# Performance work log

Hardware: AMD Instinct MI355X
Metric: run time of the kernel (lower is better)

## Reference

```python
import jax, jax.numpy as jnp
import numpy as np

D_K = 64


def setup_inputs() -> dict:
    key = jax.random.key(0)
    kq, kk, kv, km = jax.random.split(key, 4)
    B, H, S = 4, 16, 2048
    Q = jax.random.normal(kq, (B, H, S, D_K), dtype=jnp.float32)
    K = jax.random.normal(kk, (B, H, S, D_K), dtype=jnp.float32)
    V = jax.random.normal(kv, (B, H, S, D_K), dtype=jnp.float32)
    # boolean mask, True = masked out; broadcast over heads
    mask = jax.random.randint(km, (B, 1, S, S), 0, 2).astype(jnp.bool_)
    return {"Q": Q, "K": K, "V": V, "mask": mask}


def reference(Q, K, V, mask):
    scale = jnp.sqrt(jnp.asarray(D_K, dtype=Q.dtype))
    # [B,H,S,S] scores
    scores = jnp.einsum('bhqd,bhkd->bhqk', Q, K) / scale
    scores = jnp.where(mask, jnp.asarray(-1e9, dtype=scores.dtype), scores)
    attn = jax.nn.softmax(scores, axis=-1)
    return jnp.einsum('bhqk,bhkd->bhqd', attn, V)
```

## Files before the change

### kernel.cpp

```cpp
#include <hip/hip_runtime.h>
#include <hip/hip_bf16.h>


#define SEQ   2048
#define DK    64
#define NB_   4
#define NBH   64
#define KVB   64
#define QB    128
#define NT    (SEQ / KVB)

#define MASKH_WORDS ((size_t)NB_ * SEQ * 64)
#define WSK_OFF ((size_t)2 * 1024 * 1024)
#define WSV_OFF ((size_t)18 * 1024 * 1024)
#define WS_NEED ((size_t)34 * 1024 * 1024)

typedef float    f32x16 __attribute__((ext_vector_type(16)));
typedef _Float16 f16x8  __attribute__((ext_vector_type(8)));
typedef _Float16 f16x2v __attribute__((ext_vector_type(2)));

#define QSCALE 0.18033688011112042f
#define MINIT  (-1.0e4f)

#if __has_builtin(__builtin_amdgcn_exp2f)
#define EXP2F(x) __builtin_amdgcn_exp2f(x)
#else
__device__ __forceinline__ float EXP2F(float x) {
  float r;
  asm("v_exp_f32 %0, %1\n\ts_nop 1" : "=v"(r) : "v"(x));
  return r;
}
#endif

__device__ __forceinline__ unsigned pkrtz(float lo, float hi) {
  auto v = __builtin_amdgcn_cvt_pkrtz(lo, hi);
  return __builtin_bit_cast(unsigned, v);
}

#define GLOAD16(g, l)                                                          \
  __builtin_amdgcn_global_load_lds(                                            \
      (const __attribute__((address_space(1))) unsigned*)(g),                  \
      (__attribute__((address_space(3))) unsigned*)(l), 16, 0, 0)

#define BARRIER()                                          \
  do {                                                     \
    asm volatile("s_waitcnt lgkmcnt(0)" ::: "memory");     \
    __builtin_amdgcn_s_barrier();                          \
  } while (0)

__device__ __forceinline__ void halfswap(unsigned a, unsigned b,
                                         unsigned& out_lo, unsigned& out_hi, int hiL) {
#if __has_builtin(__builtin_amdgcn_permlane32_swap)
  auto r = __builtin_amdgcn_permlane32_swap(a, b, false, false);
  out_lo = r[0];
  out_hi = r[1];
#else
  unsigned ax = __shfl_xor(a, 32), bx = __shfl_xor(b, 32);
  out_lo = hiL ? bx : a;
  out_hi = hiL ? b : ax;
#endif
}

__global__ __launch_bounds__(256) void pre_all(
    const int* __restrict__ M, const float* __restrict__ K,
    const float* __restrict__ V, unsigned* __restrict__ Mh,
    _Float16* __restrict__ wsK, _Float16* __restrict__ wsV) {
  const int blk = blockIdx.x;
  if (blk < 2048) {
    int t  = blk * 256 + threadIdx.x;
    int hi = t & 1, T = (t >> 1) & 31, q = (t >> 6) & 2047, b = t >> 17;
    const int* src = M + ((size_t)b * SEQ + q) * SEQ + T * 64 + 4 * hi;
    unsigned bits = 0;
#pragma unroll
    for (int kvb = 0; kvb < 2; ++kvb)
#pragma unroll
      for (int m = 0; m < 4; ++m) {
        int4 v = *(const int4*)(src + 32 * kvb + 8 * m);
        int sh = 16 * kvb + 4 * m;
        bits |= ((unsigned)(v.x != 0) << sh) | ((unsigned)(v.y != 0) << (sh + 1)) |
                ((unsigned)(v.z != 0) << (sh + 2)) | ((unsigned)(v.w != 0) << (sh + 3));
      }
    Mh[t] = bits;
  } else if (blk < 6144) {
    int t  = (blk - 2048) * 256 + threadIdx.x;
    int lq = t & 31, c = (t >> 5) & 15, kt = (t >> 9) & 31, bh = t >> 14;
    int kv = kt * 64 + (c >> 3) * 32 + lq;
    int d0 = ((c >> 1) & 3) * 16 + (c & 1) * 8;
    const float4* src = (const float4*)(K + ((size_t)bh * SEQ + kv) * DK + d0);
    float4 a = src[0], b4 = src[1];
    uint4 o = { pkrtz(a.x, a.y), pkrtz(a.z, a.w), pkrtz(b4.x, b4.y), pkrtz(b4.z, b4.w) };
    *(uint4*)(wsK + (size_t)t * 8) = o;
  } else {
    int t  = (blk - 6144) * 256 + threadIdx.x;
    int lq = t & 31, c = (t >> 5) & 15, kt = (t >> 9) & 31, bh = t >> 14;
    int kv0 = kt * 64 + ((c >> 1) & 3) * 16 + (c & 1) * 8;
    int d   = (c >> 3) * 32 + lq;
    const float* vp = V + ((size_t)bh * SEQ + kv0) * DK + d;
    float v[8];
#pragma unroll
    for (int j = 0; j < 8; ++j) v[j] = vp[(size_t)j * DK];
    uint4 o = { pkrtz(v[0], v[1]), pkrtz(v[2], v[3]), pkrtz(v[4], v[5]), pkrtz(v[6], v[7]) };
    *(uint4*)(wsV + (size_t)t * 8) = o;
  }
}


__global__ __launch_bounds__(256) void sda_attn_pc(
    const float* __restrict__ Q, const unsigned* __restrict__ Mh,
    const _Float16* __restrict__ wsK, const _Float16* __restrict__ wsV,
    float* __restrict__ O) {
  __shared__ __align__(16) _Float16 Kl[2][16 * 256];
  __shared__ __align__(16) _Float16 Vt[2][16 * 256];

  const int bh   = blockIdx.x;
  const int qt   = blockIdx.y;
  const int b    = bh >> 4;
  const int tid  = threadIdx.x;
  const int wid  = tid >> 6;
  const int lane = tid & 63;
  const int lq   = lane & 31;
  const int hiL  = lane >> 5;

  const size_t base = (size_t)bh * SEQ * DK;
  const int    q    = qt * QB + wid * 32 + lq;

  f16x8 qf[4];
  {
    const float* qp = Q + base + (size_t)q * DK + hiL * 8;
#pragma unroll
    for (int kk = 0; kk < 4; ++kk) {
      float4 A  = *(const float4*)(qp + kk * 16);
      float4 Bv = *(const float4*)(qp + kk * 16 + 4);
      uint4 u;
      u.x = pkrtz(A.x * QSCALE, A.y * QSCALE);
      u.y = pkrtz(A.z * QSCALE, A.w * QSCALE);
      u.z = pkrtz(Bv.x * QSCALE, Bv.y * QSCALE);
      u.w = pkrtz(Bv.z * QSCALE, Bv.w * QSCALE);
      qf[kk] = __builtin_bit_cast(f16x8, u);
    }
  }

  f32x16 oacc[2];
#pragma unroll
  for (int db = 0; db < 2; ++db)
#pragma unroll
    for (int r = 0; r < 16; ++r) oacc[db][r] = 0.f;
  float lreg = 0.f;

  const _Float16* skb = wsK + (size_t)bh * 32 * 4096 + wid * 1024 + lane * 8;
  const _Float16* svb = wsV + (size_t)bh * 32 * 4096 + wid * 1024 + lane * 8;

#define STAGE_GL(buf_, kt_)                                   \
  {                                                           \
    const _Float16* sk = skb + (size_t)(kt_) * 4096;          \
    const _Float16* sv = svb + (size_t)(kt_) * 4096;          \
    _Float16* dk = &Kl[buf_][wid * 1024];                     \
    _Float16* dv = &Vt[buf_][wid * 1024];                     \
    GLOAD16(sk, dk);                                          \
    GLOAD16(sk + 512, dk + 512);                              \
    GLOAD16(sv, dv);                                          \
    GLOAD16(sv + 512, dv + 512);                              \
  }

  const unsigned* Mhp = Mh + ((size_t)b * SEQ + q) * 64 + hiL;
  const f16x2v ones = {(_Float16)1.0f, (_Float16)1.0f};
  (void)ones;

  STAGE_GL(0, 0);
  unsigned mw_cur = Mhp[0];
  asm volatile("s_waitcnt vmcnt(0)" ::: "memory");
  BARRIER();

  for (int t = 0; t < NT; ++t) {
    const int  cur  = t & 1;
    const bool more = (t + 1 < NT);
    unsigned mw_next = 0;
    if (more) {
      STAGE_GL(cur ^ 1, t + 1);
      mw_next = Mhp[2 * (t + 1)];
    }

    f32x16 sc[2];
#pragma unroll
    for (int kvb = 0; kvb < 2; ++kvb)
#pragma unroll
      for (int r = 0; r < 16; ++r)
        sc[kvb][r] = (mw_cur & (1u << (16 * kvb + r))) ? MINIT : 0.f;

    __builtin_amdgcn_s_setprio(1);
#pragma unroll
    for (int kk = 0; kk < 4; ++kk)
#pragma unroll
      for (int kvb = 0; kvb < 2; ++kvb) {
        f16x8 kf = *(const f16x8*)&Kl[cur][(kvb * 8 + kk * 2 + hiL) * 256 + lq * 8];
        sc[kvb] = __builtin_amdgcn_mfma_f32_32x32x16_f16(kf, qf[kk], sc[kvb], 0, 0, 0);
      }
    __builtin_amdgcn_s_setprio(0);

    float rs0 = 0.f, rs1 = 0.f;
    unsigned pr[2][4][2];
#pragma unroll
    for (int kvb = 0; kvb < 2; ++kvb)
#pragma unroll
      for (int m = 0; m < 4; ++m) {
        float e0 = EXP2F(sc[kvb][4 * m + 0]);
        float e1 = EXP2F(sc[kvb][4 * m + 1]);
        float e2 = EXP2F(sc[kvb][4 * m + 2]);
        float e3 = EXP2F(sc[kvb][4 * m + 3]);
        unsigned w0 = pkrtz(e0, e1);
        unsigned w1 = pkrtz(e2, e3);
        pr[kvb][m][0] = w0;
        pr[kvb][m][1] = w1;
#if __has_builtin(__builtin_amdgcn_fdot2)
        rs0 = __builtin_amdgcn_fdot2(__builtin_bit_cast(f16x2v, w0), ones, rs0, false);
        rs1 = __builtin_amdgcn_fdot2(__builtin_bit_cast(f16x2v, w1), ones, rs1, false);
#else
        rs0 += e0 + e1;
        rs1 += e2 + e3;
#endif
      }
    float rs = rs0 + rs1;

    {
      unsigned ru = __builtin_bit_cast(unsigned, rs), plo, phi;
      halfswap(ru, ru, plo, phi, hiL);
      float other = __builtin_bit_cast(float, hiL ? plo : phi);
      lreg += rs + other;
    }

#pragma unroll
    for (int ks = 0; ks < 4; ++ks) {
      const int kvb = ks >> 1, ms = (ks & 1) * 2;
      unsigned w0, w1, w2, w3;
      halfswap(pr[kvb][ms][0], pr[kvb][ms + 1][0], w0, w2, hiL);
      halfswap(pr[kvb][ms][1], pr[kvb][ms + 1][1], w1, w3, hiL);
      f16x8 pf = __builtin_bit_cast(f16x8, make_uint4(w0, w1, w2, w3));

      __builtin_amdgcn_s_setprio(1);
#pragma unroll
      for (int db = 0; db < 2; ++db) {
        f16x8 vf = *(const f16x8*)&Vt[cur][(db * 8 + ks * 2 + hiL) * 256 + lq * 8];
        oacc[db] = __builtin_amdgcn_mfma_f32_32x32x16_f16(vf, pf, oacc[db], 0, 0, 0);
      }
      __builtin_amdgcn_s_setprio(0);
    }

    mw_cur = mw_next;
    if (more) {
      asm volatile("s_waitcnt vmcnt(0)" ::: "memory");
      BARRIER();
    }
  }

  float inv = (lreg > 0.f) ? 1.0f / lreg : 0.f;
  float* op = O + base + (size_t)q * DK + 4 * hiL;
#pragma unroll
  for (int db = 0; db < 2; ++db)
#pragma unroll
    for (int m = 0; m < 4; ++m) {
      float4 o;
      o.x = oacc[db][4 * m + 0] * inv;
      o.y = oacc[db][4 * m + 1] * inv;
      o.z = oacc[db][4 * m + 2] * inv;
      o.w = oacc[db][4 * m + 3] * inv;
      *(float4*)(op + 32 * db + 8 * m) = o;
    }
}


#define CH 264
__global__ __launch_bounds__(256) void sda_attn_fb(
    const float* __restrict__ Q, const float* __restrict__ K,
    const float* __restrict__ V, const int* __restrict__ M,
    float* __restrict__ O) {
  __shared__ __align__(16) _Float16 Kl[2][16 * CH];
  __shared__ __align__(16) _Float16 Vt[2][16 * CH];
  const int bh = blockIdx.x, qt = blockIdx.y, b = bh >> 4;
  const int tid = threadIdx.x, wid = tid >> 6, lane = tid & 63;
  const int lq = lane & 31, hiL = lane >> 5;
  const size_t base = (size_t)bh * SEQ * DK;
  const int q = qt * QB + wid * 32 + lq;

  f16x8 qf[4];
  {
    const float* qp = Q + base + (size_t)q * DK + hiL * 8;
#pragma unroll
    for (int kk = 0; kk < 4; ++kk) {
      float4 A = *(const float4*)(qp + kk * 16), Bv = *(const float4*)(qp + kk * 16 + 4);
      uint4 u = { pkrtz(A.x * QSCALE, A.y * QSCALE), pkrtz(A.z * QSCALE, A.w * QSCALE),
                  pkrtz(Bv.x * QSCALE, Bv.y * QSCALE), pkrtz(Bv.z * QSCALE, Bv.w * QSCALE) };
      qf[kk] = __builtin_bit_cast(f16x8, u);
    }
  }
  f32x16 oacc[2];
#pragma unroll
  for (int db = 0; db < 2; ++db)
#pragma unroll
    for (int r = 0; r < 16; ++r) oacc[db][r] = 0.f;
  float lreg = 0.f;

  const int krow = tid >> 2, c0 = tid & 3, kp = tid & 31, d8 = (tid >> 5) * 8;
  const float* Kg = K + base + (size_t)krow * DK + c0 * 16;
  const float* Vg0 = V + base + (size_t)(2 * kp) * DK + d8;
  const float* Vg1 = Vg0 + DK;
  const int kwa = ((krow >> 5) * 8 + c0 * 2) * CH + (krow & 31) * 8;
  const int kwb = kwa + CH;
  const int vwb = ((d8 >> 5) * 8 + (kp >> 3) * 2 + ((kp >> 2) & 1)) * CH +
                  (d8 & 31) * 8 + (kp & 3) * 2;
  float4 kpre[4], vpre[4];
#define FLOADT(kb_)                                                      \
  {                                                                      \
    const float* kg = Kg + (size_t)(kb_)*DK;                             \
    _Pragma("unroll") for (int i = 0; i < 4; ++i)                        \
        kpre[i] = *(const float4*)(kg + 4 * i);                          \
    const float* va = Vg0 + (size_t)(kb_)*DK;                            \
    const float* vb = Vg1 + (size_t)(kb_)*DK;                            \
    vpre[0] = *(const float4*)va; vpre[1] = *(const float4*)(va + 4);    \
    vpre[2] = *(const float4*)vb; vpre[3] = *(const float4*)(vb + 4);    \
  }
#define FSTAGE(b_)                                                          \
  {                                                                         \
    uint4 u0, u1;                                                           \
    u0.x = pkrtz(kpre[0].x, kpre[0].y); u0.y = pkrtz(kpre[0].z, kpre[0].w); \
    u0.z = pkrtz(kpre[1].x, kpre[1].y); u0.w = pkrtz(kpre[1].z, kpre[1].w); \
    u1.x = pkrtz(kpre[2].x, kpre[2].y); u1.y = pkrtz(kpre[2].z, kpre[2].w); \
    u1.z = pkrtz(kpre[3].x, kpre[3].y); u1.w = pkrtz(kpre[3].z, kpre[3].w); \
    *(uint4*)&Kl[b_][kwa] = u0;                                             \
    *(uint4*)&Kl[b_][kwb] = u1;                                             \
    const float* va_ = (const float*)&vpre[0];                              \
    const float* vc_ = (const float*)&vpre[2];                              \
    _Pragma("unroll") for (int j = 0; j < 8; ++j)                           \
        *(unsigned*)&Vt[b_][vwb + j * 8] = pkrtz(va_[j], vc_[j]);           \
  }
  const int* Mrow = M + ((size_t)b * SEQ + q) * SEQ + 4 * hiL;
  FLOADT(0); FSTAGE(0); FLOADT(KVB);
  BARRIER();
  for (int t = 0; t < NT; ++t) {
    const int cur = t & 1;
    f32x16 sc[2];
#pragma unroll
    for (int kvb = 0; kvb < 2; ++kvb)
#pragma unroll
      for (int r = 0; r < 16; ++r) sc[kvb][r] = 0.f;
#pragma unroll
    for (int kk = 0; kk < 4; ++kk)
#pragma unroll
      for (int kvb = 0; kvb < 2; ++kvb) {
        f16x8 kf = *(const f16x8*)&Kl[cur][(kvb * 8 + kk * 2 + hiL) * CH + lq * 8];
        sc[kvb] = __builtin_amdgcn_mfma_f32_32x32x16_f16(kf, qf[kk], sc[kvb], 0, 0, 0);
      }
    const bool more = (t + 1 < NT);
    if (more) { FSTAGE(cur ^ 1); if (t + 2 < NT) FLOADT((t + 2) * KVB); }
    int4 mraw[8];
#pragma unroll
    for (int kvb = 0; kvb < 2; ++kvb)
#pragma unroll
      for (int m = 0; m < 4; ++m)
        mraw[kvb * 4 + m] = *(const int4*)(Mrow + t * KVB + 32 * kvb + 8 * m);
    float rs = 0.f;
    unsigned pr[2][4][2];
#pragma unroll
    for (int kvb = 0; kvb < 2; ++kvb) {
      float e[16];
#pragma unroll
      for (int r = 0; r < 16; ++r) {
        float ev = EXP2F(sc[kvb][r]);
        int4 v = mraw[kvb * 4 + (r >> 2)];
        int mm = (r & 3) == 0 ? v.x : (r & 3) == 1 ? v.y : (r & 3) == 2 ? v.z : v.w;
        ev = mm != 0 ? 0.f : ev;
        e[r] = ev; rs += ev;
      }
#pragma unroll
      for (int m = 0; m < 4; ++m) {
        pr[kvb][m][0] = pkrtz(e[4 * m + 0], e[4 * m + 1]);
        pr[kvb][m][1] = pkrtz(e[4 * m + 2], e[4 * m + 3]);
      }
    }
    {
      unsigned ru = __builtin_bit_cast(unsigned, rs), plo, phi;
      halfswap(ru, ru, plo, phi, hiL);
      lreg += rs + __builtin_bit_cast(float, hiL ? plo : phi);
    }
#pragma unroll
    for (int ks = 0; ks < 4; ++ks) {
      const int kvb = ks >> 1, ms = (ks & 1) * 2;
      unsigned w0, w1, w2, w3;
      halfswap(pr[kvb][ms][0], pr[kvb][ms + 1][0], w0, w2, hiL);
      halfswap(pr[kvb][ms][1], pr[kvb][ms + 1][1], w1, w3, hiL);
      f16x8 pf = __builtin_bit_cast(f16x8, make_uint4(w0, w1, w2, w3));
#pragma unroll
      for (int db = 0; db < 2; ++db) {
        f16x8 vf = *(const f16x8*)&Vt[cur][(db * 8 + ks * 2 + hiL) * CH + lq * 8];
        oacc[db] = __builtin_amdgcn_mfma_f32_32x32x16_f16(vf, pf, oacc[db], 0, 0, 0);
      }
    }
    if (more) BARRIER();
  }
  float inv = (lreg > 0.f) ? 1.0f / lreg : 0.f;
  float* op = O + base + (size_t)q * DK + 4 * hiL;
#pragma unroll
  for (int db = 0; db < 2; ++db)
#pragma unroll
    for (int m = 0; m < 4; ++m) {
      float4 o;
      o.x = oacc[db][4 * m + 0] * inv;
      o.y = oacc[db][4 * m + 1] * inv;
      o.z = oacc[db][4 * m + 2] * inv;
      o.w = oacc[db][4 * m + 3] * inv;
      *(float4*)(op + 32 * db + 8 * m) = o;
    }
}

extern "C" void kernel_launch(void* const* d_in, const int* in_sizes, int n_in,
                              void* d_out, int out_size, void* d_ws, size_t ws_size,
                              hipStream_t stream) {
  const float* Q = (const float*)d_in[0];
  const float* K = (const float*)d_in[1];
  const float* V = (const float*)d_in[2];
  const int*   M = (const int*)d_in[3];
  float*       O = (float*)d_out;
  dim3 grid(NBH, SEQ / QB);

  if (ws_size >= WS_NEED) {
    unsigned*  Mh  = (unsigned*)d_ws;
    _Float16*  wsK = (_Float16*)((char*)d_ws + WSK_OFF);
    _Float16*  wsV = (_Float16*)((char*)d_ws + WSV_OFF);
    pre_all<<<10240, 256, 0, stream>>>(M, K, V, Mh, wsK, wsV);
    sda_attn_pc<<<grid, 256, 0, stream>>>(Q, Mh, wsK, wsV, O);
  } else {
    sda_attn_fb<<<grid, 256, 0, stream>>>(Q, K, V, M, O);
  }
}
```

Baseline: 145.0 us.

## Software-pipeline QK of next tile with softmax/PV and prefetch two tiles ahead

Restructures the attention loop so the QK MFMAs for the next KV tile are issued before the exp/PV work of the current tile, using two alternating score register sets and a manually unrolled pair of iterations. Global-to-LDS staging now runs two tiles ahead with a triple-buffered V tile. Masking is applied by bitwise zeroing of the exponentials rather than seeding the accumulator with a large negative value, and the row sum uses plain float adds. This aims to overlap matrix-core work with transcendental/VALU work, at the cost of more registers and LDS.

```diff
diff --git a/kernel.cpp b/kernel.cpp
--- a/kernel.cpp
+++ b/kernel.cpp
@@ -20,7 +20,6 @@
 typedef _Float16 f16x2v __attribute__((ext_vector_type(2)));
 
 #define QSCALE 0.18033688011112042f
-#define MINIT  (-1.0e4f)
 
 #if __has_builtin(__builtin_amdgcn_exp2f)
 #define EXP2F(x) __builtin_amdgcn_exp2f(x)
@@ -35,6 +34,12 @@
 __device__ __forceinline__ unsigned pkrtz(float lo, float hi) {
   auto v = __builtin_amdgcn_cvt_pkrtz(lo, hi);
   return __builtin_bit_cast(unsigned, v);
+}
+
+__device__ __forceinline__ float mzero(float v, unsigned mw, int idx) {
+  int s = ((int)(mw << (31 - idx))) >> 31;
+  unsigned r = __builtin_bit_cast(unsigned, v) & ~(unsigned)s;
+  return __builtin_bit_cast(float, r);
 }
 
 #define GLOAD16(g, l)                                                          \
@@ -110,7 +115,7 @@
     const _Float16* __restrict__ wsK, const _Float16* __restrict__ wsV,
     float* __restrict__ O) {
   __shared__ __align__(16) _Float16 Kl[2][16 * 256];
-  __shared__ __align__(16) _Float16 Vt[2][16 * 256];
+  __shared__ __align__(16) _Float16 Vt[3][16 * 256];
 
   const int bh   = blockIdx.x;
   const int qt   = blockIdx.y;
@@ -149,107 +154,90 @@
 
   const _Float16* skb = wsK + (size_t)bh * 32 * 4096 + wid * 1024 + lane * 8;
   const _Float16* svb = wsV + (size_t)bh * 32 * 4096 + wid * 1024 + lane * 8;
-
-#define STAGE_GL(buf_, kt_)                                   \
-  {                                                           \
-    const _Float16* sk = skb + (size_t)(kt_) * 4096;          \
-    const _Float16* sv = svb + (size_t)(kt_) * 4096;          \
-    _Float16* dk = &Kl[buf_][wid * 1024];                     \
-    _Float16* dv = &Vt[buf_][wid * 1024];                     \
-    GLOAD16(sk, dk);                                          \
-    GLOAD16(sk + 512, dk + 512);                              \
-    GLOAD16(sv, dv);                                          \
-    GLOAD16(sv + 512, dv + 512);                              \
-  }
-
   const unsigned* Mhp = Mh + ((size_t)b * SEQ + q) * 64 + hiL;
   const f16x2v ones = {(_Float16)1.0f, (_Float16)1.0f};
   (void)ones;
 
-  STAGE_GL(0, 0);
-  unsigned mw_cur = Mhp[0];
+#define STAGE2(j_)                                            \
+  {                                                           \
+    const _Float16* sk = skb + (size_t)(j_) * 4096;           \
+    const _Float16* sv = svb + (size_t)(j_) * 4096;           \
+    _Float16* dk = &Kl[(j_) & 1][wid * 1024];                 \
+    _Float16* dv = &Vt[(j_) % 3][wid * 1024];                 \
+    GLOAD16(sk, dk); GLOAD16(sk + 512, dk + 512);             \
+    GLOAD16(sv, dv); GLOAD16(sv + 512, dv + 512);             \
+  }
+
+#define QKSTEP(SCN, par_)                                                         \
+  {                                                                               \
+    _Pragma("unroll") for (int kvb = 0; kvb < 2; ++kvb)                           \
+      _Pragma("unroll") for (int r = 0; r < 16; ++r) SCN[kvb][r] = 0.f;           \
+    __builtin_amdgcn_s_setprio(1);                                                \
+    _Pragma("unroll") for (int kk = 0; kk < 4; ++kk)                              \
+      _Pragma("unroll") for (int kvb = 0; kvb < 2; ++kvb) {                       \
+        f16x8 kf = *(const f16x8*)&Kl[par_][(kvb * 8 + kk * 2 + hiL) * 256 + lq * 8]; \
+        SCN[kvb] = __builtin_amdgcn_mfma_f32_32x32x16_f16(kf, qf[kk], SCN[kvb], 0, 0, 0); \
+      }                                                                           \
+    __builtin_amdgcn_s_setprio(0);                                                \
+  }
+
+#define ITER(T_, SCC, SCN, MWV)                                                   \
+  {                                                                               \
+    const int t_ = (T_);                                                          \
+    if (t_ + 2 < NT) STAGE2(t_ + 2);                                              \
+    unsigned mwt = (t_ + 2 < NT) ? Mhp[2 * (t_ + 2)] : 0u;                        \
+    if (t_ + 1 < NT) QKSTEP(SCN, (t_ + 1) & 1);                                   \
+    unsigned pr[2][4][2];                                                         \
+    {                                                                             \
+      float rs0 = 0.f, rs1 = 0.f;                                                 \
+      _Pragma("unroll") for (int kvb = 0; kvb < 2; ++kvb)                         \
+        _Pragma("unroll") for (int m = 0; m < 4; ++m) {                           \
+          float e0 = mzero(EXP2F(SCC[kvb][4 * m + 0]), MWV, 16 * kvb + 4 * m + 0);\
+          float e1 = mzero(EXP2F(SCC[kvb][4 * m + 1]), MWV, 16 * kvb + 4 * m + 1);\
+          float e2 = mzero(EXP2F(SCC[kvb][4 * m + 2]), MWV, 16 * kvb + 4 * m + 2);\
+          float e3 = mzero(EXP2F(SCC[kvb][4 * m + 3]), MWV, 16 * kvb + 4 * m + 3);\
+          unsigned w0 = pkrtz(e0, e1), w1 = pkrtz(e2, e3);                        \
+          pr[kvb][m][0] = w0; pr[kvb][m][1] = w1;                                 \
+          rs0 += e0 + e1;  rs1 += e2 + e3;                                        \
+        }                                                                         \
+      float rs = rs0 + rs1;                                                       \
+      unsigned ru = __builtin_bit_cast(unsigned, rs), plo, phi;                   \
+      halfswap(ru, ru, plo, phi, hiL);                                            \
+      lreg += rs + __builtin_bit_cast(float, hiL ? plo : phi);                    \
+    }                                                                             \
+    _Pragma("unroll") for (int ks = 0; ks < 4; ++ks) {                            \
+      const int kvb = ks >> 1, ms = (ks & 1) * 2;                                 \
+      unsigned w0, w1, w2, w3;                                                    \
+      halfswap(pr[kvb][ms][0], pr[kvb][ms + 1][0], w0, w2, hiL);                  \
+      halfswap(pr[kvb][ms][1], pr[kvb][ms + 1][1], w1, w3, hiL);                  \
+      f16x8 pf = __builtin_bit_cast(f16x8, make_uint4(w0, w1, w2, w3));           \
+      __builtin_amdgcn_s_setprio(1);                                              \
+      _Pragma("unroll") for (int db = 0; db < 2; ++db) {                          \
+        f16x8 vf = *(const f16x8*)&Vt[t_ % 3][(db * 8 + ks * 2 + hiL) * 256 + lq * 8]; \
+        oacc[db] = __builtin_amdgcn_mfma_f32_32x32x16_f16(vf, pf, oacc[db], 0, 0, 0); \
+      }                                                                           \
+      __builtin_amdgcn_s_setprio(0);                                              \
+    }                                                                             \
+    MWV = mwt;                                                                    \
+    if (t_ + 1 < NT) {                                                            \
+      asm volatile("s_waitcnt vmcnt(0)" ::: "memory");                            \
+      BARRIER();                                                                  \
+    }                                                                             \
+  }
+
+  STAGE2(0);
+  STAGE2(1);
+  unsigned mwA = Mhp[0], mwB = Mhp[2];
   asm volatile("s_waitcnt vmcnt(0)" ::: "memory");
   BARRIER();
 
-  for (int t = 0; t < NT; ++t) {
-    const int  cur  = t & 1;
-    const bool more = (t + 1 < NT);
-    unsigned mw_next = 0;
-    if (more) {
-      STAGE_GL(cur ^ 1, t + 1);
-      mw_next = Mhp[2 * (t + 1)];
-    }
-
-    f32x16 sc[2];
-#pragma unroll
-    for (int kvb = 0; kvb < 2; ++kvb)
-#pragma unroll
-      for (int r = 0; r < 16; ++r)
-        sc[kvb][r] = (mw_cur & (1u << (16 * kvb + r))) ? MINIT : 0.f;
-
-    __builtin_amdgcn_s_setprio(1);
-#pragma unroll
-    for (int kk = 0; kk < 4; ++kk)
-#pragma unroll
-      for (int kvb = 0; kvb < 2; ++kvb) {
-        f16x8 kf = *(const f16x8*)&Kl[cur][(kvb * 8 + kk * 2 + hiL) * 256 + lq * 8];
-        sc[kvb] = __builtin_amdgcn_mfma_f32_32x32x16_f16(kf, qf[kk], sc[kvb], 0, 0, 0);
-      }
-    __builtin_amdgcn_s_setprio(0);
-
-    float rs0 = 0.f, rs1 = 0.f;
-    unsigned pr[2][4][2];
-#pragma unroll
-    for (int kvb = 0; kvb < 2; ++kvb)
-#pragma unroll
-      for (int m = 0; m < 4; ++m) {
-        float e0 = EXP2F(sc[kvb][4 * m + 0]);
-        float e1 = EXP2F(sc[kvb][4 * m + 1]);
-        float e2 = EXP2F(sc[kvb][4 * m + 2]);
-        float e3 = EXP2F(sc[kvb][4 * m + 3]);
-        unsigned w0 = pkrtz(e0, e1);
-        unsigned w1 = pkrtz(e2, e3);
-        pr[kvb][m][0] = w0;
-        pr[kvb][m][1] = w1;
-#if __has_builtin(__builtin_amdgcn_fdot2)
-        rs0 = __builtin_amdgcn_fdot2(__builtin_bit_cast(f16x2v, w0), ones, rs0, false);
-        rs1 = __builtin_amdgcn_fdot2(__builtin_bit_cast(f16x2v, w1), ones, rs1, false);
-#else
-        rs0 += e0 + e1;
-        rs1 += e2 + e3;
-#endif
-      }
-    float rs = rs0 + rs1;
-
-    {
-      unsigned ru = __builtin_bit_cast(unsigned, rs), plo, phi;
-      halfswap(ru, ru, plo, phi, hiL);
-      float other = __builtin_bit_cast(float, hiL ? plo : phi);
-      lreg += rs + other;
-    }
-
-#pragma unroll
-    for (int ks = 0; ks < 4; ++ks) {
-      const int kvb = ks >> 1, ms = (ks & 1) * 2;
-      unsigned w0, w1, w2, w3;
-      halfswap(pr[kvb][ms][0], pr[kvb][ms + 1][0], w0, w2, hiL);
-      halfswap(pr[kvb][ms][1], pr[kvb][ms + 1][1], w1, w3, hiL);
-      f16x8 pf = __builtin_bit_cast(f16x8, make_uint4(w0, w1, w2, w3));
-
-      __builtin_amdgcn_s_setprio(1);
-#pragma unroll
-      for (int db = 0; db < 2; ++db) {
-        f16x8 vf = *(const f16x8*)&Vt[cur][(db * 8 + ks * 2 + hiL) * 256 + lq * 8];
-        oacc[db] = __builtin_amdgcn_mfma_f32_32x32x16_f16(vf, pf, oacc[db], 0, 0, 0);
-      }
-      __builtin_amdgcn_s_setprio(0);
-    }
-
-    mw_cur = mw_next;
-    if (more) {
-      asm volatile("s_waitcnt vmcnt(0)" ::: "memory");
-      BARRIER();
-    }
+  f32x16 scA[2], scB[2];
+  QKSTEP(scA, 0);
+  BARRIER();
+
+  for (int tt = 0; tt < NT; tt += 2) {
+    ITER(tt,     scA, scB, mwA);
+    ITER(tt + 1, scB, scA, mwB);
   }
 
   float inv = (lreg > 0.f) ? 1.0f / lreg : 0.f;
@@ -273,8 +261,8 @@
     const float* __restrict__ Q, const float* __restrict__ K,
     const float* __restrict__ V, const int* __restrict__ M,
     float* __restrict__ O) {
-  __shared__ __align__(16) _Float16 Kl[2][16 * CH];
-  __shared__ __align__(16) _Float16 Vt[2][16 * CH];
+  __shared__ __align__(16) _Float16 Klf[2][16 * CH];
+  __shared__ __align__(16) _Float16 Vtf[2][16 * CH];
   const int bh = blockIdx.x, qt = blockIdx.y, b = bh >> 4;
   const int tid = threadIdx.x, wid = tid >> 6, lane = tid & 63;
   const int lq = lane & 31, hiL = lane >> 5;
@@ -325,12 +313,12 @@
     u0.z = pkrtz(kpre[1].x, kpre[1].y); u0.w = pkrtz(kpre[1].z, kpre[1].w); \
     u1.x = pkrtz(kpre[2].x, kpre[2].y); u1.y = pkrtz(kpre[2].z, kpre[2].w); \
     u1.z = pkrtz(kpre[3].x, kpre[3].y); u1.w = pkrtz(kpre[3].z, kpre[3].w); \
-    *(uint4*)&Kl[b_][kwa] = u0;                                             \
-    *(uint4*)&Kl[b_][kwb] = u1;                                             \
+    *(uint4*)&Klf[b_][kwa] = u0;                                            \
+    *(uint4*)&Klf[b_][kwb] = u1;                                            \
     const float* va_ = (const float*)&vpre[0];                              \
     const float* vc_ = (const float*)&vpre[2];                              \
     _Pragma("unroll") for (int j = 0; j < 8; ++j)                           \
-        *(unsigned*)&Vt[b_][vwb + j * 8] = pkrtz(va_[j], vc_[j]);           \
+        *(unsigned*)&Vtf[b_][vwb + j * 8] = pkrtz(va_[j], vc_[j]);          \
   }
   const int* Mrow = M + ((size_t)b * SEQ + q) * SEQ + 4 * hiL;
   FLOADT(0); FSTAGE(0); FLOADT(KVB);
@@ -346,7 +334,7 @@
     for (int kk = 0; kk < 4; ++kk)
 #pragma unroll
       for (int kvb = 0; kvb < 2; ++kvb) {
-        f16x8 kf = *(const f16x8*)&Kl[cur][(kvb * 8 + kk * 2 + hiL) * CH + lq * 8];
+        f16x8 kf = *(const f16x8*)&Klf[cur][(kvb * 8 + kk * 2 + hiL) * CH + lq * 8];
         sc[kvb] = __builtin_amdgcn_mfma_f32_32x32x16_f16(kf, qf[kk], sc[kvb], 0, 0, 0);
       }
     const bool more = (t + 1 < NT);
@@ -390,7 +378,7 @@
       f16x8 pf = __builtin_bit_cast(f16x8, make_uint4(w0, w1, w2, w3));
 #pragma unroll
       for (int db = 0; db < 2; ++db) {
-        f16x8 vf = *(const f16x8*)&Vt[cur][(db * 8 + ks * 2 + hiL) * CH + lq * 8];
+        f16x8 vf = *(const f16x8*)&Vtf[cur][(db * 8 + ks * 2 + hiL) * CH + lq * 8];
         oacc[db] = __builtin_amdgcn_mfma_f32_32x32x16_f16(vf, pf, oacc[db], 0, 0, 0);
       }
     }
```

Result: no change. 144.6 us (-0.2%).

## Replace LDS-staged attention with single-wave blocks loading K/V fragments into registers

Applied to the files above, without the earlier changes.

The main attention kernel drops LDS staging and block barriers. It becomes one 64-thread wave per 32-query block, loading K and V MFMA fragments straight from the pre-swizzled fp16 workspace into registers, with next-tile prefetch issued inside the loop. Masking now zeroes exp results with a bitmask AND instead of preloading -1e4 into the score accumulators. This removes barrier and LDS traffic, but it loses sharing of K/V tiles across the four waves, so global/L2 traffic per query rises, and register pressure grows from holding two tiles of fragments.

```diff
diff --git a/kernel.cpp b/kernel.cpp
--- a/kernel.cpp
+++ b/kernel.cpp
@@ -7,7 +7,6 @@
 #define NB_   4
 #define NBH   64
 #define KVB   64
-#define QB    128
 #define NT    (SEQ / KVB)
 
 #define MASKH_WORDS ((size_t)NB_ * SEQ * 64)
@@ -20,7 +19,6 @@
 typedef _Float16 f16x2v __attribute__((ext_vector_type(2)));
 
 #define QSCALE 0.18033688011112042f
-#define MINIT  (-1.0e4f)
 
 #if __has_builtin(__builtin_amdgcn_exp2f)
 #define EXP2F(x) __builtin_amdgcn_exp2f(x)
@@ -37,16 +35,11 @@
   return __builtin_bit_cast(unsigned, v);
 }
 
-#define GLOAD16(g, l)                                                          \
-  __builtin_amdgcn_global_load_lds(                                            \
-      (const __attribute__((address_space(1))) unsigned*)(g),                  \
-      (__attribute__((address_space(3))) unsigned*)(l), 16, 0, 0)
-
-#define BARRIER()                                          \
-  do {                                                     \
-    asm volatile("s_waitcnt lgkmcnt(0)" ::: "memory");     \
-    __builtin_amdgcn_s_barrier();                          \
-  } while (0)
+__device__ __forceinline__ float mzero(float v, unsigned mw, int idx) {
+  int s = ((int)(mw << (31 - idx))) >> 31;
+  unsigned r = __builtin_bit_cast(unsigned, v) & ~(unsigned)s;
+  return __builtin_bit_cast(float, r);
+}
 
 __device__ __forceinline__ void halfswap(unsigned a, unsigned b,
                                          unsigned& out_lo, unsigned& out_hi, int hiL) {
@@ -105,24 +98,20 @@
 }
 
 
-__global__ __launch_bounds__(256) void sda_attn_pc(
+__global__ __launch_bounds__(64) void sda_attn_reg(
     const float* __restrict__ Q, const unsigned* __restrict__ Mh,
     const _Float16* __restrict__ wsK, const _Float16* __restrict__ wsV,
     float* __restrict__ O) {
-  __shared__ __align__(16) _Float16 Kl[2][16 * 256];
-  __shared__ __align__(16) _Float16 Vt[2][16 * 256];
-
-  const int bh   = blockIdx.x;
-  const int qt   = blockIdx.y;
+  const int blk  = blockIdx.x;
+  const int bh   = blk >> 6;
+  const int w    = blk & 63;
   const int b    = bh >> 4;
-  const int tid  = threadIdx.x;
-  const int wid  = tid >> 6;
-  const int lane = tid & 63;
+  const int lane = threadIdx.x;
   const int lq   = lane & 31;
   const int hiL  = lane >> 5;
 
   const size_t base = (size_t)bh * SEQ * DK;
-  const int    q    = qt * QB + wid * 32 + lq;
+  const int    q    = w * 32 + lq;
 
   f16x8 qf[4];
   {
@@ -147,55 +136,54 @@
     for (int r = 0; r < 16; ++r) oacc[db][r] = 0.f;
   float lreg = 0.f;
 
-  const _Float16* skb = wsK + (size_t)bh * 32 * 4096 + wid * 1024 + lane * 8;
-  const _Float16* svb = wsV + (size_t)bh * 32 * 4096 + wid * 1024 + lane * 8;
-
-#define STAGE_GL(buf_, kt_)                                   \
-  {                                                           \
-    const _Float16* sk = skb + (size_t)(kt_) * 4096;          \
-    const _Float16* sv = svb + (size_t)(kt_) * 4096;          \
-    _Float16* dk = &Kl[buf_][wid * 1024];                     \
-    _Float16* dv = &Vt[buf_][wid * 1024];                     \
-    GLOAD16(sk, dk);                                          \
-    GLOAD16(sk + 512, dk + 512);                              \
-    GLOAD16(sv, dv);                                          \
-    GLOAD16(sv + 512, dv + 512);                              \
-  }
-
+  const _Float16* kp  = wsK + (size_t)bh * 32 * 4096 + (size_t)hiL * 256 + (size_t)lq * 8;
+  const _Float16* vp  = wsV + (size_t)bh * 32 * 4096 + (size_t)hiL * 256 + (size_t)lq * 8;
   const unsigned* Mhp = Mh + ((size_t)b * SEQ + q) * 64 + hiL;
+
+  f16x8 kfr[8], vfr[8];
+
+#define LOADKF(t_)                                                        \
+  {                                                                       \
+    const _Float16* s_ = kp + (size_t)(t_) * 4096;                        \
+    _Pragma("unroll") for (int kvb = 0; kvb < 2; ++kvb)                   \
+      _Pragma("unroll") for (int kk = 0; kk < 4; ++kk)                    \
+        kfr[kvb * 4 + kk] = *(const f16x8*)(s_ + kvb * 2048 + kk * 512);  \
+  }
+#define LOADVF(t_)                                                        \
+  {                                                                       \
+    const _Float16* s_ = vp + (size_t)(t_) * 4096;                        \
+    _Pragma("unroll") for (int ks = 0; ks < 4; ++ks)                      \
+      _Pragma("unroll") for (int db = 0; db < 2; ++db)                    \
+        vfr[ks * 2 + db] = *(const f16x8*)(s_ + db * 2048 + ks * 512);    \
+  }
+
   const f16x2v ones = {(_Float16)1.0f, (_Float16)1.0f};
   (void)ones;
 
-  STAGE_GL(0, 0);
-  unsigned mw_cur = Mhp[0];
-  asm volatile("s_waitcnt vmcnt(0)" ::: "memory");
-  BARRIER();
+  LOADKF(0);
+  LOADVF(0);
+  unsigned mw = Mhp[0];
 
   for (int t = 0; t < NT; ++t) {
-    const int  cur  = t & 1;
-    const bool more = (t + 1 < NT);
-    unsigned mw_next = 0;
-    if (more) {
-      STAGE_GL(cur ^ 1, t + 1);
-      mw_next = Mhp[2 * (t + 1)];
-    }
+    const int tn = (t + 1 < NT) ? t + 1 : t;
 
     f32x16 sc[2];
 #pragma unroll
     for (int kvb = 0; kvb < 2; ++kvb)
 #pragma unroll
-      for (int r = 0; r < 16; ++r)
-        sc[kvb][r] = (mw_cur & (1u << (16 * kvb + r))) ? MINIT : 0.f;
+      for (int r = 0; r < 16; ++r) sc[kvb][r] = 0.f;
 
     __builtin_amdgcn_s_setprio(1);
 #pragma unroll
     for (int kk = 0; kk < 4; ++kk)
 #pragma unroll
-      for (int kvb = 0; kvb < 2; ++kvb) {
-        f16x8 kf = *(const f16x8*)&Kl[cur][(kvb * 8 + kk * 2 + hiL) * 256 + lq * 8];
-        sc[kvb] = __builtin_amdgcn_mfma_f32_32x32x16_f16(kf, qf[kk], sc[kvb], 0, 0, 0);
-      }
+      for (int kvb = 0; kvb < 2; ++kvb)
+        sc[kvb] = __builtin_amdgcn_mfma_f32_32x32x16_f16(kfr[kvb * 4 + kk], qf[kk],
+                                                         sc[kvb], 0, 0, 0);
     __builtin_amdgcn_s_setprio(0);
+
+    LOADKF(tn);
+    unsigned mwn = Mhp[2 * tn];
 
     float rs0 = 0.f, rs1 = 0.f;
     unsigned pr[2][4][2];
@@ -203,12 +191,11 @@
     for (int kvb = 0; kvb < 2; ++kvb)
 #pragma unroll
       for (int m = 0; m < 4; ++m) {
-        float e0 = EXP2F(sc[kvb][4 * m + 0]);
-        float e1 = EXP2F(sc[kvb][4 * m + 1]);
-        float e2 = EXP2F(sc[kvb][4 * m + 2]);
-        float e3 = EXP2F(sc[kvb][4 * m + 3]);
-        unsigned w0 = pkrtz(e0, e1);
-        unsigned w1 = pkrtz(e2, e3);
+        float e0 = mzero(EXP2F(sc[kvb][4 * m + 0]), mw, 16 * kvb + 4 * m + 0);
+        float e1 = mzero(EXP2F(sc[kvb][4 * m + 1]), mw, 16 * kvb + 4 * m + 1);
+        float e2 = mzero(EXP2F(sc[kvb][4 * m + 2]), mw, 16 * kvb + 4 * m + 2);
+        float e3 = mzero(EXP2F(sc[kvb][4 * m + 3]), mw, 16 * kvb + 4 * m + 3);
+        unsigned w0 = pkrtz(e0, e1), w1 = pkrtz(e2, e3);
         pr[kvb][m][0] = w0;
         pr[kvb][m][1] = w1;
 #if __has_builtin(__builtin_amdgcn_fdot2)
@@ -219,13 +206,11 @@
         rs1 += e2 + e3;
 #endif
       }
-    float rs = rs0 + rs1;
-
     {
+      float rs = rs0 + rs1;
       unsigned ru = __builtin_bit_cast(unsigned, rs), plo, phi;
       halfswap(ru, ru, plo, phi, hiL);
-      float other = __builtin_bit_cast(float, hiL ? plo : phi);
-      lreg += rs + other;
+      lreg += rs + __builtin_bit_cast(float, hiL ? plo : phi);
     }
 
 #pragma unroll
@@ -238,18 +223,14 @@
 
       __builtin_amdgcn_s_setprio(1);
 #pragma unroll
-      for (int db = 0; db < 2; ++db) {
-        f16x8 vf = *(const f16x8*)&Vt[cur][(db * 8 + ks * 2 + hiL) * 256 + lq * 8];
-        oacc[db] = __builtin_amdgcn_mfma_f32_32x32x16_f16(vf, pf, oacc[db], 0, 0, 0);
-      }
+      for (int db = 0; db < 2; ++db)
+        oacc[db] = __builtin_amdgcn_mfma_f32_32x32x16_f16(vfr[ks * 2 + db], pf,
+                                                          oacc[db], 0, 0, 0);
       __builtin_amdgcn_s_setprio(0);
     }
 
-    mw_cur = mw_next;
-    if (more) {
-      asm volatile("s_waitcnt vmcnt(0)" ::: "memory");
-      BARRIER();
-    }
+    LOADVF(tn);
+    mw = mwn;
   }
 
   float inv = (lreg > 0.f) ? 1.0f / lreg : 0.f;
@@ -269,17 +250,24 @@
 
 
 #define CH 264
+#define QB 128
 __global__ __launch_bounds__(256) void sda_attn_fb(
     const float* __restrict__ Q, const float* __restrict__ K,
     const float* __restrict__ V, const int* __restrict__ M,
     float* __restrict__ O) {
-  __shared__ __align__(16) _Float16 Kl[2][16 * CH];
-  __shared__ __align__(16) _Float16 Vt[2][16 * CH];
+  __shared__ __align__(16) _Float16 Klf[2][16 * CH];
+  __shared__ __align__(16) _Float16 Vtf[2][16 * CH];
   const int bh = blockIdx.x, qt = blockIdx.y, b = bh >> 4;
   const int tid = threadIdx.x, wid = tid >> 6, lane = tid & 63;
   const int lq = lane & 31, hiL = lane >> 5;
   const size_t base = (size_t)bh * SEQ * DK;
   const int q = qt * QB + wid * 32 + lq;
+
+#define BARRIER()                                          \
+  do {                                                     \
+    asm volatile("s_waitcnt lgkmcnt(0)" ::: "memory");     \
+    __builtin_amdgcn_s_barrier();                          \
+  } while (0)
 
   f16x8 qf[4];
   {
@@ -325,12 +313,12 @@
     u0.z = pkrtz(kpre[1].x, kpre[1].y); u0.w = pkrtz(kpre[1].z, kpre[1].w); \
     u1.x = pkrtz(kpre[2].x, kpre[2].y); u1.y = pkrtz(kpre[2].z, kpre[2].w); \
     u1.z = pkrtz(kpre[3].x, kpre[3].y); u1.w = pkrtz(kpre[3].z, kpre[3].w); \
-    *(uint4*)&Kl[b_][kwa] = u0;                                             \
-    *(uint4*)&Kl[b_][kwb] = u1;                                             \
+    *(uint4*)&Klf[b_][kwa] = u0;                                            \
+    *(uint4*)&Klf[b_][kwb] = u1;                                            \
     const float* va_ = (const float*)&vpre[0];                              \
     const float* vc_ = (const float*)&vpre[2];                              \
     _Pragma("unroll") for (int j = 0; j < 8; ++j)                           \
-        *(unsigned*)&Vt[b_][vwb + j * 8] = pkrtz(va_[j], vc_[j]);           \
+        *(unsigned*)&Vtf[b_][vwb + j * 8] = pkrtz(va_[j], vc_[j]);          \
   }
   const int* Mrow = M + ((size_t)b * SEQ + q) * SEQ + 4 * hiL;
   FLOADT(0); FSTAGE(0); FLOADT(KVB);
@@ -346,7 +334,7 @@
     for (int kk = 0; kk < 4; ++kk)
 #pragma unroll
       for (int kvb = 0; kvb < 2; ++kvb) {
-        f16x8 kf = *(const f16x8*)&Kl[cur][(kvb * 8 + kk * 2 + hiL) * CH + lq * 8];
+        f16x8 kf = *(const f16x8*)&Klf[cur][(kvb * 8 + kk * 2 + hiL) * CH + lq * 8];
         sc[kvb] = __builtin_amdgcn_mfma_f32_32x32x16_f16(kf, qf[kk], sc[kvb], 0, 0, 0);
       }
     const bool more = (t + 1 < NT);
@@ -390,7 +378,7 @@
       f16x8 pf = __builtin_bit_cast(f16x8, make_uint4(w0, w1, w2, w3));
 #pragma unroll
       for (int db = 0; db < 2; ++db) {
-        f16x8 vf = *(const f16x8*)&Vt[cur][(db * 8 + ks * 2 + hiL) * CH + lq * 8];
+        f16x8 vf = *(const f16x8*)&Vtf[cur][(db * 8 + ks * 2 + hiL) * CH + lq * 8];
         oacc[db] = __builtin_amdgcn_mfma_f32_32x32x16_f16(vf, pf, oacc[db], 0, 0, 0);
       }
     }
@@ -419,15 +407,15 @@
   const float* V = (const float*)d_in[2];
   const int*   M = (const int*)d_in[3];
   float*       O = (float*)d_out;
-  dim3 grid(NBH, SEQ / QB);
 
   if (ws_size >= WS_NEED) {
     unsigned*  Mh  = (unsigned*)d_ws;
     _Float16*  wsK = (_Float16*)((char*)d_ws + WSK_OFF);
     _Float16*  wsV = (_Float16*)((char*)d_ws + WSV_OFF);
     pre_all<<<10240, 256, 0, stream>>>(M, K, V, Mh, wsK, wsV);
-    sda_attn_pc<<<grid, 256, 0, stream>>>(Q, Mh, wsK, wsV, O);
+    sda_attn_reg<<<NBH * 64, 64, 0, stream>>>(Q, Mh, wsK, wsV, O);
   } else {
+    dim3 grid(NBH, SEQ / QB);
     sda_attn_fb<<<grid, 256, 0, stream>>>(Q, K, V, M, O);
   }
 }
```

Measured after the change: 154.4 us. 1.06x slower.
